# Optimization experiments

Hardware: AMD Instinct MI355X
Metric: run time of the kernel (lower is better)

The kernel has to match this reference:

```python
import jax, jax.numpy as jnp
import numpy as np

B, P, CIN, PS = 8192, 9, 12, 64   # batch, patches, channels, patch_size
D_IN = CIN * PS                    # 768 flattened patch features
ENC_H, D = 512, 1024               # patch_encoder_hidden, embedding_dim
E, EXP_H, C = 8, 2048, 1000        # num_experts, expert hidden, num_classes
SYM, SYM_H = 6, 64                 # symbolic_dim, symbolic gating hidden


def setup_inputs() -> dict:
    key = jax.random.key(0)
    ks = jax.random.split(key, 16)
    g = lambda k, shape, fan: jax.random.normal(k, shape, jnp.float32) / np.sqrt(fan)
    return {
        "patches": jax.random.normal(ks[0], (B, P, CIN, PS), jnp.float32),
        "symbolic_features": jax.random.normal(ks[1], (B, SYM), jnp.float32),
        # patch encoder (2-layer MLP per patch)
        "enc_w1": g(ks[2], (D_IN, ENC_H), D_IN), "enc_b1": jnp.zeros((ENC_H,), jnp.float32),
        "enc_w2": g(ks[3], (ENC_H, D), ENC_H),   "enc_b2": jnp.zeros((D,), jnp.float32),
        # neural gating: Linear(D,D)-ReLU-Linear(D,E)
        "gn_w1": g(ks[4], (D, D), D), "gn_b1": jnp.zeros((D,), jnp.float32),
        "gn_w2": g(ks[5], (D, E), D), "gn_b2": jnp.zeros((E,), jnp.float32),
        # symbolic gating: Linear(SYM,64)-ReLU-Linear(64,E)
        "gs_w1": g(ks[6], (SYM, SYM_H), SYM),  "gs_b1": jnp.zeros((SYM_H,), jnp.float32),
        "gs_w2": g(ks[7], (SYM_H, E), SYM_H),  "gs_b2": jnp.zeros((E,), jnp.float32),
        # stacked experts: Linear(D,H)-ReLU-(Dropout=eval identity)-Linear(H,C)
        "ew1": g(ks[8], (E, D, EXP_H), D),      "eb1": jnp.zeros((E, EXP_H), jnp.float32),
        "ew2": g(ks[9], (E, EXP_H, C), EXP_H),  "eb2": jnp.zeros((E, C), jnp.float32),
    }


def reference(patches, symbolic_features, enc_w1, enc_b1, enc_w2, enc_b2,
              gn_w1, gn_b1, gn_w2, gn_b2, gs_w1, gs_b1, gs_w2, gs_b2,
              ew1, eb1, ew2, eb2):
    b = patches.shape[0]
    # patch encoder: (b, P, CIN*PS) -> (b, P, D)
    x = patches.reshape(b, P, D_IN)
    h = jax.nn.relu(jnp.einsum('bpf,fh->bph', x, enc_w1) + enc_b1)
    encoded = jnp.einsum('bph,hd->bpd', h, enc_w2) + enc_b2
    # mean aggregation over patches
    agg = encoded.mean(axis=1)  # (b, D)
    # symbolic gating: 0.5*neural + 0.5*symbolic logits, softmax
    neural = jax.nn.relu(agg @ gn_w1 + gn_b1) @ gn_w2 + gn_b2            # (b, E)
    symb = jax.nn.relu(symbolic_features @ gs_w1 + gs_b1) @ gs_w2 + gs_b2  # (b, E)
    gating_weights = jax.nn.softmax(0.5 * neural + 0.5 * symb, axis=1)
    # all experts densely (batched over expert axis)
    eh = jax.nn.relu(jnp.einsum('bd,edh->beh', agg, ew1) + eb1)          # (b, E, H)
    expert_logits = jnp.einsum('beh,ehc->bec', eh, ew2) + eb2            # (b, E, C)
    # gate-weighted sum
    logits = jnp.einsum('be,bec->bc', gating_weights, expert_logits)     # (b, C)
    return logits, gating_weights, expert_logits
```

## Files before the change

kernel.cpp:

```cpp
#include <hip/hip_runtime.h>
#include <hip/hip_bf16.h>

typedef __attribute__((ext_vector_type(8))) short s16x8;
typedef __attribute__((ext_vector_type(4))) float f32x4;

#define DEV __device__ __forceinline__

DEV short f2b(float f) {
  __hip_bfloat16 h = __float2bfloat16(f);
  short s; __builtin_memcpy(&s, &h, 2); return s;
}
DEV float b2f(short s) {
  __hip_bfloat16 h; __builtin_memcpy(&h, &s, 2); return __bfloat162float(h);
}

typedef __attribute__((address_space(1))) const void gvoid;
typedef __attribute__((address_space(3))) void lvoid;
DEV void gload_lds16(const void* g, void* l) {
  __builtin_amdgcn_global_load_lds((gvoid*)g, (lvoid*)l, 16, 0, 0);
}

static constexpr int kB = 8192, kP = 9, kDIN = 768, kENCH = 512, kD = 1024;
static constexpr int kE = 8, kH = 2048, kC = 1000;
static constexpr size_t OUT_GATE   = (size_t)kB * kC;
static constexpr size_t OUT_EL     = OUT_GATE + (size_t)kB * kE;

static constexpr size_t W1T  = 0;
static constexpr size_t W2T  = W1T  + 786432;
static constexpr size_t GW1T = W2T  + 1048576;
static constexpr size_t EW1T = GW1T + 2097152;
static constexpr size_t EW2T = EW1T + 33554432;
static constexpr size_t PBF  = EW2T + 32768000;
static constexpr size_t HBUF = PBF  + 113246208;
static constexpr size_t EH4  = HBUF + 75497472;
static constexpr size_t HMEAN = PBF;
static constexpr size_t AGG   = HMEAN + 8388608;
static constexpr size_t GH    = AGG   + 16777216;
static constexpr size_t NEU   = GH    + 16777216;
static constexpr size_t SYMB  = NEU   + 262144;

__global__ void cast_bf16_kernel(const float* __restrict__ in, short* __restrict__ out, size_t n8) {
  size_t i = (size_t)blockIdx.x * blockDim.x + threadIdx.x;
  if (i >= n8) return;
  float4 a = ((const float4*)in)[i * 2];
  float4 b = ((const float4*)in)[i * 2 + 1];
  s16x8 v;
  v[0] = f2b(a.x); v[1] = f2b(a.y); v[2] = f2b(a.z); v[3] = f2b(a.w);
  v[4] = f2b(b.x); v[5] = f2b(b.y); v[6] = f2b(b.z); v[7] = f2b(b.w);
  *(s16x8*)(out + i * 8) = v;
}

__global__ void transpose_cast_kernel(const float* __restrict__ in, short* __restrict__ out,
                                      int R, int C, size_t istride, size_t ostride) {
  __shared__ float tile[32][33];
  const float* W = in + istride * blockIdx.z;
  short* T = out + ostride * blockIdx.z;
  int tx = threadIdx.x, ty = threadIdx.y;
  int c0 = blockIdx.x * 32, r0 = blockIdx.y * 32;
  #pragma unroll
  for (int i = 0; i < 32; i += 8) {
    int r = r0 + ty + i, c = c0 + tx;
    if (r < R && c < C) tile[ty + i][tx] = W[(size_t)r * C + c];
  }
  __syncthreads();
  #pragma unroll
  for (int i = 0; i < 32; i += 8) {
    int rr = c0 + ty + i, cc = r0 + tx;
    if (rr < C && cc < R) T[(size_t)rr * R + cc] = f2b(tile[tx][ty + i]);
  }
}

#define BARR() __builtin_amdgcn_s_barrier()
#define LGKM0() do { asm volatile("s_waitcnt lgkmcnt(0)" ::: "memory"); \
                     __builtin_amdgcn_sched_barrier(0); } while (0)
#define VMW6() asm volatile("s_waitcnt vmcnt(6)" ::: "memory")
#define VMW4() asm volatile("s_waitcnt vmcnt(4)" ::: "memory")
#define VMW0() asm volatile("s_waitcnt vmcnt(0)" ::: "memory")

template<bool RELU, bool F32OUT, bool NTAIL>
__global__ __launch_bounds__(512, 2)
void gemm256_kernel(const short* __restrict__ A, const short* __restrict__ Bt,
                    const float* __restrict__ bias, void* __restrict__ Cout,
                    int M, int N, int K, int ldc,
                    long aZ, long bZ, long biasZ, long cZ) {
  __shared__ short Abuf[2][2][8192];
  __shared__ short Bbuf[2][2][8192];
  const int z = blockIdx.z;
  A += (size_t)z * aZ; Bt += (size_t)z * bZ; bias += (size_t)z * biasZ;

  const int XT = gridDim.x;
  int lid = blockIdx.y * XT + blockIdx.x;
  const int cpx = (XT * gridDim.y) >> 3;
  lid = (lid & 7) * cpx + (lid >> 3);
  const int bx = lid % XT, by = lid / XT;
  const int bM = by * 256, bN = bx * 256;

  const int t = threadIdx.x, lane = t & 63, wid = t >> 6;
  const int wm = wid & 1, wn = wid >> 1;
  const int lr = lane & 15, kg = lane >> 4;
  const int nkt = K >> 6;

  const int srB = t >> 3;
  const int sx = (t & 7) ^ (srB & 7);
  const int ldsoff = wid * 512;

  int ar0 = bM + srB, ar1 = bM + 64 + srB, ar2 = bM + 128 + srB, ar3 = bM + 192 + srB;
  int br0 = bN + srB, br1 = bN + 64 + srB, br2 = bN + 128 + srB, br3 = bN + 192 + srB;
  if (NTAIL) {
    if (br0 >= N) br0 = N - 1;
    if (br1 >= N) br1 = N - 1;
    if (br2 >= N) br2 = N - 1;
    if (br3 >= N) br3 = N - 1;
  }
  const short* pA00 = A + (size_t)ar0 * K + sx * 8;
  const short* pA01 = A + (size_t)ar1 * K + sx * 8;
  const short* pA10 = A + (size_t)ar2 * K + sx * 8;
  const short* pA11 = A + (size_t)ar3 * K + sx * 8;
  const short* pB00 = Bt + (size_t)br0 * K + sx * 8;
  const short* pB01 = Bt + (size_t)br1 * K + sx * 8;
  const short* pB10 = Bt + (size_t)br2 * K + sx * 8;
  const short* pB11 = Bt + (size_t)br3 * K + sx * 8;

#define STAGE_A0(tile_) do { if ((tile_) < nkt) { int par_ = (tile_) & 1; \
    gload_lds16(pA00, &Abuf[par_][0][ldsoff]); \
    gload_lds16(pA01, &Abuf[par_][0][4096 + ldsoff]); \
    pA00 += 64; pA01 += 64; } } while (0)
#define STAGE_A1(tile_) do { if ((tile_) < nkt) { int par_ = (tile_) & 1; \
    gload_lds16(pA10, &Abuf[par_][1][ldsoff]); \
    gload_lds16(pA11, &Abuf[par_][1][4096 + ldsoff]); \
    pA10 += 64; pA11 += 64; } } while (0)
#define STAGE_B0(tile_) do { if ((tile_) < nkt) { int par_ = (tile_) & 1; \
    gload_lds16(pB00, &Bbuf[par_][0][ldsoff]); \
    gload_lds16(pB01, &Bbuf[par_][0][4096 + ldsoff]); \
    pB00 += 64; pB01 += 64; } } while (0)
#define STAGE_B1(tile_) do { if ((tile_) < nkt) { int par_ = (tile_) & 1; \
    gload_lds16(pB10, &Bbuf[par_][1][ldsoff]); \
    gload_lds16(pB11, &Bbuf[par_][1][4096 + ldsoff]); \
    pB10 += 64; pB11 += 64; } } while (0)

  const int aro = (wm * 64 + lr) * 64;
  const int bro = (wn * 32 + lr) * 64;
  const int so0 = ((0 * 4 + kg) ^ (lr & 7)) * 8;
  const int so1 = ((1 * 4 + kg) ^ (lr & 7)) * 8;

  s16x8 a0[4][2], a1[4][2], b0[2][2], b1[2][2];
#define LDA0(par_) do { _Pragma("unroll") \
    for (int m_ = 0; m_ < 4; ++m_) { \
      a0[m_][0] = *(const s16x8*)&Abuf[par_][0][aro + m_ * 1024 + so0]; \
      a0[m_][1] = *(const s16x8*)&Abuf[par_][0][aro + m_ * 1024 + so1]; \
    } } while (0)
#define LDA1(par_) do { _Pragma("unroll") \
    for (int m_ = 0; m_ < 4; ++m_) { \
      a1[m_][0] = *(const s16x8*)&Abuf[par_][1][aro + m_ * 1024 + so0]; \
      a1[m_][1] = *(const s16x8*)&Abuf[par_][1][aro + m_ * 1024 + so1]; \
    } } while (0)
#define LDB0(par_) do { _Pragma("unroll") \
    for (int n_ = 0; n_ < 2; ++n_) { \
      b0[n_][0] = *(const s16x8*)&Bbuf[par_][0][bro + n_ * 1024 + so0]; \
      b0[n_][1] = *(const s16x8*)&Bbuf[par_][0][bro + n_ * 1024 + so1]; \
    } } while (0)
#define LDB1(par_) do { _Pragma("unroll") \
    for (int n_ = 0; n_ < 2; ++n_) { \
      b1[n_][0] = *(const s16x8*)&Bbuf[par_][1][bro + n_ * 1024 + so0]; \
      b1[n_][1] = *(const s16x8*)&Bbuf[par_][1][bro + n_ * 1024 + so1]; \
    } } while (0)

  f32x4 acc[2][2][4][2];
  #pragma unroll
  for (int a_ = 0; a_ < 2; ++a_)
    #pragma unroll
    for (int b_ = 0; b_ < 2; ++b_)
      #pragma unroll
      for (int m_ = 0; m_ < 4; ++m_)
        #pragma unroll
        for (int n_ = 0; n_ < 2; ++n_) acc[a_][b_][m_][n_] = (f32x4){0.f, 0.f, 0.f, 0.f};

#define MMAQ(mh, nh, AF, BF) do { \
    __builtin_amdgcn_s_setprio(1); \
    _Pragma("unroll") \
    for (int m_ = 0; m_ < 4; ++m_) \
      _Pragma("unroll") \
      for (int n_ = 0; n_ < 2; ++n_) { \
        acc[mh][nh][m_][n_] = __builtin_amdgcn_mfma_f32_16x16x32_bf16(AF[m_][0], BF[n_][0], acc[mh][nh][m_][n_], 0, 0, 0); \
        acc[mh][nh][m_][n_] = __builtin_amdgcn_mfma_f32_16x16x32_bf16(AF[m_][1], BF[n_][1], acc[mh][nh][m_][n_], 0, 0, 0); \
      } \
    __builtin_amdgcn_s_setprio(0); } while (0)

  STAGE_A0(0); STAGE_B0(0); STAGE_B1(0); STAGE_A1(0);
  VMW4();
  STAGE_A0(1); STAGE_B0(1); STAGE_B1(1);
  VMW6();
  BARR();

  for (int g = 0; g < nkt; ++g) {
    const int par = g & 1;
    LDA0(par); LDB0(par);
    STAGE_A1(g + 1);
    BARR(); LGKM0();
    MMAQ(0, 0, a0, b0);
    BARR();
    LDB1(par);
    STAGE_A0(g + 2);
    BARR(); LGKM0();
    MMAQ(0, 1, a0, b1);
    BARR();
    LDA1(par);
    STAGE_B0(g + 2);
    BARR(); LGKM0();
    MMAQ(1, 1, a1, b1);
    BARR();
    STAGE_B1(g + 2);
    if (g == nkt - 2) { VMW0(); } else if (g < nkt - 2) { VMW6(); }
    BARR(); LGKM0();
    MMAQ(1, 0, a1, b0);
    BARR();
  }

  #pragma unroll
  for (int nh = 0; nh < 2; ++nh)
    #pragma unroll
    for (int n_ = 0; n_ < 2; ++n_) {
      int col = bN + nh * 128 + wn * 32 + n_ * 16 + lr;
      if (NTAIL && col >= N) continue;
      float bv = bias[col];
      #pragma unroll
      for (int mh = 0; mh < 2; ++mh)
        #pragma unroll
        for (int m_ = 0; m_ < 4; ++m_) {
          int row0 = bM + mh * 128 + wm * 64 + m_ * 16 + kg * 4;
          #pragma unroll
          for (int r_ = 0; r_ < 4; ++r_) {
            float v = acc[mh][nh][m_][n_][r_] + bv;
            if (RELU) v = fmaxf(v, 0.f);
            size_t off = (size_t)(row0 + r_) * ldc + col;
            if (F32OUT) ((float*)Cout + (size_t)z * cZ)[off] = v;
            else        ((short*)Cout + (size_t)z * cZ)[off] = f2b(v);
          }
        }
    }
#undef STAGE_A0
#undef STAGE_A1
#undef STAGE_B0
#undef STAGE_B1
#undef LDA0
#undef LDA1
#undef LDB0
#undef LDB1
#undef MMAQ
}

template<bool RELU, bool F32OUT>
__global__ __launch_bounds__(256, 2)
void gemm_bt_kernel(const short* __restrict__ A, const short* __restrict__ Bt,
                    const float* __restrict__ bias, void* __restrict__ Cout,
                    int M, int N, int K, int ldc) {
  __shared__ short As[128 * 32];
  __shared__ short Bs[128 * 32];
  const int t = threadIdx.x;
  const int lane = t & 63, wid = t >> 6;
  const int wr = wid >> 1, wc = wid & 1;
  const int lr = lane & 15, lk8 = (lane >> 4) * 8;
  const int arow0 = blockIdx.y * 128;
  const int bcol0 = blockIdx.x * 128;

  f32x4 acc[4][4];
  #pragma unroll
  for (int m = 0; m < 4; ++m)
    #pragma unroll
    for (int n = 0; n < 4; ++n) acc[m][n] = (f32x4){0.f, 0.f, 0.f, 0.f};

  const int srow = t >> 2, sseg = (t & 3) * 8;
  const short* ga0 = A + (size_t)(arow0 + srow) * K + sseg;
  const short* ga1 = ga0 + (size_t)64 * K;
  int br0 = bcol0 + srow;      if (br0 >= N) br0 = N - 1;
  int br1 = bcol0 + srow + 64; if (br1 >= N) br1 = N - 1;
  const short* gb0 = Bt + (size_t)br0 * K + sseg;
  const short* gb1 = Bt + (size_t)br1 * K + sseg;
  short* lA0 = As + wid * 512;
  short* lA1 = As + 2048 + wid * 512;
  short* lB0 = Bs + wid * 512;
  short* lB1 = Bs + 2048 + wid * 512;

  for (int k0 = 0; k0 < K; k0 += 32) {
    __syncthreads();
    gload_lds16(ga0, lA0);
    gload_lds16(ga1, lA1);
    gload_lds16(gb0, lB0);
    gload_lds16(gb1, lB1);
    ga0 += 32; ga1 += 32; gb0 += 32; gb1 += 32;
    __syncthreads();
    s16x8 af[4], bfr[4];
    #pragma unroll
    for (int m = 0; m < 4; ++m) af[m] = *(const s16x8*)&As[(wr * 64 + m * 16 + lr) * 32 + lk8];
    #pragma unroll
    for (int n = 0; n < 4; ++n) bfr[n] = *(const s16x8*)&Bs[(wc * 64 + n * 16 + lr) * 32 + lk8];
    #pragma unroll
    for (int m = 0; m < 4; ++m)
      #pragma unroll
      for (int n = 0; n < 4; ++n)
        acc[m][n] = __builtin_amdgcn_mfma_f32_16x16x32_bf16(af[m], bfr[n], acc[m][n], 0, 0, 0);
  }

  #pragma unroll
  for (int n = 0; n < 4; ++n) {
    int col = bcol0 + wc * 64 + n * 16 + lr;
    if (col >= N) continue;
    float bv = bias[col];
    #pragma unroll
    for (int m = 0; m < 4; ++m) {
      int row0 = arow0 + wr * 64 + m * 16 + (lane >> 4) * 4;
      #pragma unroll
      for (int r = 0; r < 4; ++r) {
        float v = acc[m][n][r] + bv;
        if (RELU) v = fmaxf(v, 0.f);
        size_t off = (size_t)(row0 + r) * ldc + col;
        if (F32OUT) ((float*)Cout)[off] = v;
        else        ((short*)Cout)[off] = f2b(v);
      }
    }
  }
}

__global__ void mean9_kernel(const short* __restrict__ h, short* __restrict__ hm) {
  size_t i = (size_t)blockIdx.x * blockDim.x + threadIdx.x;
  if (i >= (size_t)kB * kENCH / 8) return;
  size_t b = i >> 6; int d8 = (int)(i & 63);
  const short* base = h + b * kP * kENCH + d8 * 8;
  float s[8] = {0, 0, 0, 0, 0, 0, 0, 0};
  #pragma unroll
  for (int p = 0; p < kP; ++p) {
    s16x8 v = *(const s16x8*)(base + p * kENCH);
    #pragma unroll
    for (int j = 0; j < 8; ++j) s[j] += b2f(v[j]);
  }
  s16x8 o;
  #pragma unroll
  for (int j = 0; j < 8; ++j) o[j] = f2b(s[j] * (1.f / 9.f));
  *(s16x8*)(hm + i * 8) = o;
}

__global__ __launch_bounds__(256)
void gating_neural_kernel(const short* __restrict__ gh, const float* __restrict__ w2,
                          const float* __restrict__ b2, float* __restrict__ neural) {
  int wid = threadIdx.x >> 6, lane = threadIdx.x & 63;
  int row = blockIdx.x * 4 + wid;
  float acc[8] = {0,0,0,0,0,0,0,0};
  const short* grow = gh + (size_t)row * kD;
  for (int k = lane; k < kD; k += 64) {
    float x = b2f(grow[k]);
    const float* w = w2 + (size_t)k * 8;
    #pragma unroll
    for (int c = 0; c < 8; ++c) acc[c] += x * w[c];
  }
  #pragma unroll
  for (int c = 0; c < 8; ++c)
    #pragma unroll
    for (int off = 32; off >= 1; off >>= 1) acc[c] += __shfl_xor(acc[c], off);
  if (lane == 0) {
    #pragma unroll
    for (int c = 0; c < 8; ++c) neural[(size_t)row * 8 + c] = acc[c] + b2[c];
  }
}

__global__ __launch_bounds__(256)
void gating_symb_kernel(const float* __restrict__ sym, const float* __restrict__ w1,
                        const float* __restrict__ b1, const float* __restrict__ w2,
                        const float* __restrict__ b2, float* __restrict__ symb) {
  int wid = threadIdx.x >> 6, lane = threadIdx.x & 63;
  int row = blockIdx.x * 4 + wid;
  float s0 = sym[(size_t)row * 6 + 0], s1 = sym[(size_t)row * 6 + 1], s2 = sym[(size_t)row * 6 + 2];
  float s3 = sym[(size_t)row * 6 + 3], s4 = sym[(size_t)row * 6 + 4], s5 = sym[(size_t)row * 6 + 5];
  float hh = b1[lane];
  hh += s0 * w1[0 * 64 + lane] + s1 * w1[1 * 64 + lane] + s2 * w1[2 * 64 + lane];
  hh += s3 * w1[3 * 64 + lane] + s4 * w1[4 * 64 + lane] + s5 * w1[5 * 64 + lane];
  hh = fmaxf(hh, 0.f);
  float acc[8];
  #pragma unroll
  for (int c = 0; c < 8; ++c) acc[c] = hh * w2[lane * 8 + c];
  #pragma unroll
  for (int c = 0; c < 8; ++c)
    #pragma unroll
    for (int off = 32; off >= 1; off >>= 1) acc[c] += __shfl_xor(acc[c], off);
  if (lane == 0) {
    #pragma unroll
    for (int c = 0; c < 8; ++c) symb[(size_t)row * 8 + c] = acc[c] + b2[c];
  }
}

__global__ void gating_softmax_kernel(const float* __restrict__ neural, const float* __restrict__ symb,
                                      float* __restrict__ gate_out) {
  int row = blockIdx.x * blockDim.x + threadIdx.x;
  if (row >= kB) return;
  float g[8], m = -1e30f;
  #pragma unroll
  for (int c = 0; c < 8; ++c) {
    g[c] = 0.5f * (neural[(size_t)row * 8 + c] + symb[(size_t)row * 8 + c]);
    m = fmaxf(m, g[c]);
  }
  float sum = 0.f;
  #pragma unroll
  for (int c = 0; c < 8; ++c) { g[c] = expf(g[c] - m); sum += g[c]; }
  float inv = 1.f / sum;
  #pragma unroll
  for (int c = 0; c < 8; ++c) gate_out[(size_t)row * 8 + c] = g[c] * inv;
}

__global__ __launch_bounds__(256)
void combine_kernel(float* __restrict__ out) {
  int b = blockIdx.y;
  int c = blockIdx.x * 256 + threadIdx.x;
  __shared__ float g[8];
  if (threadIdx.x < 8) g[threadIdx.x] = out[OUT_GATE + (size_t)b * 8 + threadIdx.x];
  __syncthreads();
  if (c < kC) {
    const float* el = out + OUT_EL + (size_t)b * (kE * kC) + c;
    float a = 0.f;
    #pragma unroll
    for (int e = 0; e < 8; ++e) a += g[e] * el[e * kC];
    out[(size_t)b * kC + c] = a;
  }
}

static void launch_gemm128(bool relu, bool f32out, const short* A, const short* Bt, const float* bias,
                           void* C, int M, int N, int K, int ldc, hipStream_t s) {
  dim3 g((N + 127) / 128, M / 128), b(256);
  if (relu && !f32out)       gemm_bt_kernel<true,  false><<<g, b, 0, s>>>(A, Bt, bias, C, M, N, K, ldc);
  else if (!relu && !f32out) gemm_bt_kernel<false, false><<<g, b, 0, s>>>(A, Bt, bias, C, M, N, K, ldc);
  else if (relu && f32out)   gemm_bt_kernel<true,  true ><<<g, b, 0, s>>>(A, Bt, bias, C, M, N, K, ldc);
  else                       gemm_bt_kernel<false, true ><<<g, b, 0, s>>>(A, Bt, bias, C, M, N, K, ldc);
}

extern "C" void kernel_launch(void* const* d_in, const int* in_sizes, int n_in,
                              void* d_out, int out_size, void* d_ws, size_t ws_size,
                              hipStream_t stream) {
  const float* patches = (const float*)d_in[0];
  const float* symf    = (const float*)d_in[1];
  const float* enc_w1  = (const float*)d_in[2];
  const float* enc_b1  = (const float*)d_in[3];
  const float* enc_w2  = (const float*)d_in[4];
  const float* enc_b2  = (const float*)d_in[5];
  const float* gn_w1   = (const float*)d_in[6];
  const float* gn_b1   = (const float*)d_in[7];
  const float* gn_w2   = (const float*)d_in[8];
  const float* gn_b2   = (const float*)d_in[9];
  const float* gs_w1   = (const float*)d_in[10];
  const float* gs_b1   = (const float*)d_in[11];
  const float* gs_w2   = (const float*)d_in[12];
  const float* gs_b2   = (const float*)d_in[13];
  const float* ew1     = (const float*)d_in[14];
  const float* eb1     = (const float*)d_in[15];
  const float* ew2     = (const float*)d_in[16];
  const float* eb2     = (const float*)d_in[17];
  char* ws = (char*)d_ws;
  float* out = (float*)d_out;
  dim3 tb(32, 8);

  {
    size_t n8 = (size_t)kB * kP * kDIN / 8;
    cast_bf16_kernel<<<(unsigned)((n8 + 255) / 256), 256, 0, stream>>>(patches, (short*)(ws + PBF), n8);
  }
  transpose_cast_kernel<<<dim3(16, 24, 1), tb, 0, stream>>>(enc_w1, (short*)(ws + W1T),  kDIN,  kENCH, 0, 0);
  transpose_cast_kernel<<<dim3(32, 16, 1), tb, 0, stream>>>(enc_w2, (short*)(ws + W2T),  kENCH, kD,    0, 0);
  transpose_cast_kernel<<<dim3(32, 32, 1), tb, 0, stream>>>(gn_w1,  (short*)(ws + GW1T), kD,    kD,    0, 0);
  transpose_cast_kernel<<<dim3(64, 32, 8), tb, 0, stream>>>(ew1,    (short*)(ws + EW1T), kD,    kH,
                                                            (size_t)kD * kH, (size_t)kD * kH);
  transpose_cast_kernel<<<dim3(32, 64, 8), tb, 0, stream>>>(ew2,    (short*)(ws + EW2T), kH,    kC,
                                                            (size_t)kH * kC, (size_t)kH * kC);
  gemm256_kernel<true, false, false><<<dim3(2, 288, 1), 512, 0, stream>>>(
      (short*)(ws + PBF), (short*)(ws + W1T), enc_b1, ws + HBUF,
      kB * kP, kENCH, kDIN, kENCH, 0, 0, 0, 0);
  mean9_kernel<<<(kB * kENCH / 8) / 256, 256, 0, stream>>>((short*)(ws + HBUF), (short*)(ws + HMEAN));
  launch_gemm128(false, false, (short*)(ws + HMEAN), (short*)(ws + W2T), enc_b2,
                 ws + AGG, kB, kD, kENCH, kD, stream);
  launch_gemm128(true, false, (short*)(ws + AGG), (short*)(ws + GW1T), gn_b1,
                 ws + GH, kB, kD, kD, kD, stream);
  gating_neural_kernel<<<kB / 4, 256, 0, stream>>>((short*)(ws + GH), gn_w2, gn_b2, (float*)(ws + NEU));
  gating_symb_kernel<<<kB / 4, 256, 0, stream>>>(symf, gs_w1, gs_b1, gs_w2, gs_b2, (float*)(ws + SYMB));
  gating_softmax_kernel<<<kB / 256, 256, 0, stream>>>((float*)(ws + NEU), (float*)(ws + SYMB), out + OUT_GATE);
  for (int h = 0; h < 2; ++h) {
    int e0 = h * 4;
    gemm256_kernel<true, false, false><<<dim3(8, 32, 4), 512, 0, stream>>>(
        (short*)(ws + AGG), (short*)(ws + EW1T) + (size_t)e0 * kH * kD, eb1 + (size_t)e0 * kH,
        ws + EH4, kB, kH, kD, kH,
        0, (long)kH * kD, kH, (long)kB * kH);
    gemm256_kernel<false, true, true><<<dim3(4, 32, 4), 512, 0, stream>>>(
        (short*)(ws + EH4), (short*)(ws + EW2T) + (size_t)e0 * kC * kH, eb2 + (size_t)e0 * kC,
        out + OUT_EL + (size_t)e0 * kC, kB, kC, kH, kE * kC,
        (long)kB * kH, (long)kC * kH, kC, kC);
  }
  combine_kernel<<<dim3(4, kB), 256, 0, stream>>>(out);
}
```

Before: 1.016 ms.

## Remap 256x256 GEMM warp layout and reorder stage/fragment pipeline

Changes the warp-to-tile mapping in the 256x256 GEMM so each warp covers 128 contiguous rows and 64 contiguous columns, with new LDS fragment offsets that reuse a single A fragment buffer across two B fragments. The global-to-LDS prefetch schedule is reordered: fewer tiles are prestaged, stage issue is interleaved differently with the four MFMA quarters, and vmcnt waits change from 6 to 4. A partial lgkmcnt(8) wait is added and the sched_barrier after the lgkm waits is dropped, giving the compiler more scheduling freedom. The goal is to cut register pressure and improve overlap of loads with MFMA, at the risk of changed LDS bank patterns and ordering hazards.

```diff
diff --git a/kernel.cpp b/kernel.cpp
--- a/kernel.cpp
+++ b/kernel.cpp
@@ -71,9 +71,8 @@
 }
 
 #define BARR() __builtin_amdgcn_s_barrier()
-#define LGKM0() do { asm volatile("s_waitcnt lgkmcnt(0)" ::: "memory"); \
-                     __builtin_amdgcn_sched_barrier(0); } while (0)
-#define VMW6() asm volatile("s_waitcnt vmcnt(6)" ::: "memory")
+#define LGKM0() asm volatile("s_waitcnt lgkmcnt(0)" ::: "memory")
+#define LGKM8() asm volatile("s_waitcnt lgkmcnt(8)" ::: "memory")
 #define VMW4() asm volatile("s_waitcnt vmcnt(4)" ::: "memory")
 #define VMW0() asm volatile("s_waitcnt vmcnt(0)" ::: "memory")
 
@@ -96,7 +95,7 @@
   const int bM = by * 256, bN = bx * 256;
 
   const int t = threadIdx.x, lane = t & 63, wid = t >> 6;
-  const int wm = wid & 1, wn = wid >> 1;
+  const int wm = wid >> 2, wn = wid & 3;
   const int lr = lane & 15, kg = lane >> 4;
   const int nkt = K >> 6;
 
@@ -104,7 +103,6 @@
   const int sx = (t & 7) ^ (srB & 7);
   const int ldsoff = wid * 512;
 
-  int ar0 = bM + srB, ar1 = bM + 64 + srB, ar2 = bM + 128 + srB, ar3 = bM + 192 + srB;
   int br0 = bN + srB, br1 = bN + 64 + srB, br2 = bN + 128 + srB, br3 = bN + 192 + srB;
   if (NTAIL) {
     if (br0 >= N) br0 = N - 1;
@@ -112,10 +110,10 @@
     if (br2 >= N) br2 = N - 1;
     if (br3 >= N) br3 = N - 1;
   }
-  const short* pA00 = A + (size_t)ar0 * K + sx * 8;
-  const short* pA01 = A + (size_t)ar1 * K + sx * 8;
-  const short* pA10 = A + (size_t)ar2 * K + sx * 8;
-  const short* pA11 = A + (size_t)ar3 * K + sx * 8;
+  const short* pA00 = A + (size_t)(bM + srB) * K + sx * 8;
+  const short* pA01 = A + (size_t)(bM + 64 + srB) * K + sx * 8;
+  const short* pA10 = A + (size_t)(bM + 128 + srB) * K + sx * 8;
+  const short* pA11 = A + (size_t)(bM + 192 + srB) * K + sx * 8;
   const short* pB00 = Bt + (size_t)br0 * K + sx * 8;
   const short* pB01 = Bt + (size_t)br1 * K + sx * 8;
   const short* pB10 = Bt + (size_t)br2 * K + sx * 8;
@@ -138,31 +136,22 @@
     gload_lds16(pB11, &Bbuf[par_][1][4096 + ldsoff]); \
     pB10 += 64; pB11 += 64; } } while (0)
 
-  const int aro = (wm * 64 + lr) * 64;
-  const int bro = (wn * 32 + lr) * 64;
-  const int so0 = ((0 * 4 + kg) ^ (lr & 7)) * 8;
-  const int so1 = ((1 * 4 + kg) ^ (lr & 7)) * 8;
-
-  s16x8 a0[4][2], a1[4][2], b0[2][2], b1[2][2];
-#define LDA0(par_) do { _Pragma("unroll") \
+  const int aro = lr * 64;
+  const int bro = ((wn & 1) * 64 + lr) * 64;
+  const int bh = wn >> 1;
+  const int so0 = (kg ^ (lr & 7)) * 8;
+  const int so1 = ((4 + kg) ^ (lr & 7)) * 8;
+
+  s16x8 a[4][2], b0[2][2], b1[2][2];
+#define LDA(qr, par_) do { _Pragma("unroll") \
     for (int m_ = 0; m_ < 4; ++m_) { \
-      a0[m_][0] = *(const s16x8*)&Abuf[par_][0][aro + m_ * 1024 + so0]; \
-      a0[m_][1] = *(const s16x8*)&Abuf[par_][0][aro + m_ * 1024 + so1]; \
+      a[m_][0] = *(const s16x8*)&Abuf[par_][wm][(qr) * 4096 + aro + m_ * 1024 + so0]; \
+      a[m_][1] = *(const s16x8*)&Abuf[par_][wm][(qr) * 4096 + aro + m_ * 1024 + so1]; \
     } } while (0)
-#define LDA1(par_) do { _Pragma("unroll") \
-    for (int m_ = 0; m_ < 4; ++m_) { \
-      a1[m_][0] = *(const s16x8*)&Abuf[par_][1][aro + m_ * 1024 + so0]; \
-      a1[m_][1] = *(const s16x8*)&Abuf[par_][1][aro + m_ * 1024 + so1]; \
-    } } while (0)
-#define LDB0(par_) do { _Pragma("unroll") \
+#define LDB(qc, BF, par_) do { _Pragma("unroll") \
     for (int n_ = 0; n_ < 2; ++n_) { \
-      b0[n_][0] = *(const s16x8*)&Bbuf[par_][0][bro + n_ * 1024 + so0]; \
-      b0[n_][1] = *(const s16x8*)&Bbuf[par_][0][bro + n_ * 1024 + so1]; \
-    } } while (0)
-#define LDB1(par_) do { _Pragma("unroll") \
-    for (int n_ = 0; n_ < 2; ++n_) { \
-      b1[n_][0] = *(const s16x8*)&Bbuf[par_][1][bro + n_ * 1024 + so0]; \
-      b1[n_][1] = *(const s16x8*)&Bbuf[par_][1][bro + n_ * 1024 + so1]; \
+      BF[n_][0] = *(const s16x8*)&Bbuf[par_][bh][bro + (qc) * 2048 + n_ * 1024 + so0]; \
+      BF[n_][1] = *(const s16x8*)&Bbuf[par_][bh][bro + (qc) * 2048 + n_ * 1024 + so1]; \
     } } while (0)
 
   f32x4 acc[2][2][4][2];
@@ -175,62 +164,62 @@
         #pragma unroll
         for (int n_ = 0; n_ < 2; ++n_) acc[a_][b_][m_][n_] = (f32x4){0.f, 0.f, 0.f, 0.f};
 
-#define MMAQ(mh, nh, AF, BF) do { \
+#define MMAQ(qr, qc, BF) do { \
     __builtin_amdgcn_s_setprio(1); \
     _Pragma("unroll") \
     for (int m_ = 0; m_ < 4; ++m_) \
       _Pragma("unroll") \
       for (int n_ = 0; n_ < 2; ++n_) { \
-        acc[mh][nh][m_][n_] = __builtin_amdgcn_mfma_f32_16x16x32_bf16(AF[m_][0], BF[n_][0], acc[mh][nh][m_][n_], 0, 0, 0); \
-        acc[mh][nh][m_][n_] = __builtin_amdgcn_mfma_f32_16x16x32_bf16(AF[m_][1], BF[n_][1], acc[mh][nh][m_][n_], 0, 0, 0); \
+        acc[qr][qc][m_][n_] = __builtin_amdgcn_mfma_f32_16x16x32_bf16(a[m_][0], BF[n_][0], acc[qr][qc][m_][n_], 0, 0, 0); \
+        acc[qr][qc][m_][n_] = __builtin_amdgcn_mfma_f32_16x16x32_bf16(a[m_][1], BF[n_][1], acc[qr][qc][m_][n_], 0, 0, 0); \
       } \
     __builtin_amdgcn_s_setprio(0); } while (0)
 
   STAGE_A0(0); STAGE_B0(0); STAGE_B1(0); STAGE_A1(0);
+  STAGE_B0(1); STAGE_A0(1);
   VMW4();
-  STAGE_A0(1); STAGE_B0(1); STAGE_B1(1);
-  VMW6();
   BARR();
 
   for (int g = 0; g < nkt; ++g) {
     const int par = g & 1;
-    LDA0(par); LDB0(par);
+    LDA(0, par); LDB(0, b0, par);
+    STAGE_B1(g + 1);
+    LGKM8();
+    BARR(); LGKM0();
+    MMAQ(0, 0, b0);
+    BARR();
+    LDB(1, b1, par);
     STAGE_A1(g + 1);
     BARR(); LGKM0();
-    MMAQ(0, 0, a0, b0);
+    MMAQ(0, 1, b1);
     BARR();
-    LDB1(par);
+    LDA(1, par);
+    STAGE_B0(g + 2);
+    BARR(); LGKM0();
+    MMAQ(1, 1, b1);
+    BARR();
     STAGE_A0(g + 2);
     BARR(); LGKM0();
-    MMAQ(0, 1, a0, b1);
+    MMAQ(1, 0, b0);
+    if (g == nkt - 2) { VMW0(); } else if (g < nkt - 2) { VMW4(); }
     BARR();
-    LDA1(par);
-    STAGE_B0(g + 2);
-    BARR(); LGKM0();
-    MMAQ(1, 1, a1, b1);
-    BARR();
-    STAGE_B1(g + 2);
-    if (g == nkt - 2) { VMW0(); } else if (g < nkt - 2) { VMW6(); }
-    BARR(); LGKM0();
-    MMAQ(1, 0, a1, b0);
-    BARR();
-  }
-
-  #pragma unroll
-  for (int nh = 0; nh < 2; ++nh)
+  }
+
+  #pragma unroll
+  for (int qc = 0; qc < 2; ++qc)
     #pragma unroll
     for (int n_ = 0; n_ < 2; ++n_) {
-      int col = bN + nh * 128 + wn * 32 + n_ * 16 + lr;
+      int col = bN + wn * 64 + qc * 32 + n_ * 16 + lr;
       if (NTAIL && col >= N) continue;
       float bv = bias[col];
       #pragma unroll
-      for (int mh = 0; mh < 2; ++mh)
+      for (int qr = 0; qr < 2; ++qr)
         #pragma unroll
         for (int m_ = 0; m_ < 4; ++m_) {
-          int row0 = bM + mh * 128 + wm * 64 + m_ * 16 + kg * 4;
+          int row0 = bM + wm * 128 + qr * 64 + m_ * 16 + kg * 4;
           #pragma unroll
           for (int r_ = 0; r_ < 4; ++r_) {
-            float v = acc[mh][nh][m_][n_][r_] + bv;
+            float v = acc[qr][qc][m_][n_][r_] + bv;
             if (RELU) v = fmaxf(v, 0.f);
             size_t off = (size_t)(row0 + r_) * ldc + col;
             if (F32OUT) ((float*)Cout + (size_t)z * cZ)[off] = v;
@@ -242,10 +231,8 @@
 #undef STAGE_A1
 #undef STAGE_B0
 #undef STAGE_B1
-#undef LDA0
-#undef LDA1
-#undef LDB0
-#undef LDB1
+#undef LDA
+#undef LDB
 #undef MMAQ
 }
 
```

After: 1.060 ms. 1.04x slower.
